# Performance work log

Hardware: AMD Instinct MI355X
Metric: run time of the kernel (lower is better)

Reference implementation:

```python
import jax, jax.numpy as jnp
import numpy as np

N, E, D, H, FF = 50000, 800000, 128, 8, 512
DK = D // H
NTYPES = 5
EPS = 1e-5


def setup_inputs() -> dict:
    key = jax.random.key(0)
    ks = jax.random.split(key, 8)
    x = jax.random.normal(ks[0], (N, D), jnp.float32)
    edges = jax.random.randint(ks[1], (2, E), 0, N)
    etype = jax.random.randint(ks[2], (E,), 0, NTYPES)
    masks = etype[None, :] == jnp.arange(NTYPES)[:, None]  # [5, E] bool, exact partition
    s = 1.0 / np.sqrt(D)
    Wk = jax.random.normal(ks[3], (NTYPES, D, D), jnp.float32) * s
    bk = jnp.zeros((NTYPES, D), jnp.float32)
    ln1_g = jnp.ones((D,), jnp.float32)
    ln1_b = jnp.zeros((D,), jnp.float32)
    ln2_g = jnp.ones((D,), jnp.float32)
    ln2_b = jnp.zeros((D,), jnp.float32)
    W1 = jax.random.normal(ks[4], (D, FF), jnp.float32) * s
    b1 = jnp.zeros((FF,), jnp.float32)
    W2 = jax.random.normal(ks[5], (FF, D), jnp.float32) * (1.0 / np.sqrt(FF))
    b2 = jnp.zeros((D,), jnp.float32)
    return {"x": x, "edges": edges, "masks": masks, "Wk": Wk, "bk": bk,
            "ln1_g": ln1_g, "ln1_b": ln1_b, "ln2_g": ln2_g, "ln2_b": ln2_b,
            "W1": W1, "b1": b1, "W2": W2, "b2": b2}


def _layernorm(x, g, b):
    mu = x.mean(-1, keepdims=True)
    var = x.var(-1, keepdims=True)
    return (x - mu) * jax.lax.rsqrt(var + EPS) * g + b


def _proj(z, idx, masks, W, b):
    # per-edge-type masked linear: output[mask_i] = x[idx[mask_i]] @ W_i + b_i
    g = z[idx]  # [E, D] gather
    out = jnp.zeros((g.shape[0], D), z.dtype)
    for i in range(NTYPES):
        out = out + jnp.where(masks[i][:, None], g @ W[i] + b[i], 0.0)
    return out.reshape(-1, H, DK)  # [E, H, d_k]


def reference(x, edges, masks, Wk, bk, ln1_g, ln1_b, ln2_g, ln2_b, W1, b1, W2, b2):
    src, dst = edges[0], edges[1]
    n = x.shape[0]
    z = _layernorm(x, ln1_g, ln1_b)
    # source module uses self.key projection for query, key AND value
    q = _proj(z, src, masks, Wk, bk)   # [E, H, d_k]
    k = _proj(z, dst, masks, Wk, bk)   # [E, H, d_k]
    v = k                              # value = key(z, edges[1]) == key, reuse
    logits = (q * k).sum(2, keepdims=True)  # [E, H, 1], unscaled as in source
    m = jax.ops.segment_max(jax.lax.stop_gradient(logits), src, num_segments=n)
    scores = jnp.exp(logits - m[src])
    den = jax.ops.segment_sum(scores, src, num_segments=n)
    scores = scores / den[src]
    attn = jax.ops.segment_sum(scores * v, src, num_segments=n).reshape(n, -1)  # [N, D]
    x = x + attn
    z2 = _layernorm(x, ln2_g, ln2_b)
    ff = jax.nn.relu(z2 @ W1 + b1) @ W2 + b2
    return x + ff
```

## Files before the change

### kernel.cpp

```cpp
#include <hip/hip_runtime.h>

#define D 128
#define H 8
#define DK 16
#define FFDIM 512
#define NTYPES 5
#define LN_EPS 1e-5f

typedef __bf16 bf16x8 __attribute__((ext_vector_type(8)));
typedef float f32x4 __attribute__((ext_vector_type(4)));
typedef unsigned short ushort_t;
typedef unsigned int uint_t;

__device__ inline ushort_t bfbits(float f) {
  __bf16 b = (__bf16)f;
  return __builtin_bit_cast(ushort_t, b);
}

__global__ void detect_kernel(const unsigned char* __restrict__ m8, int E,
                              int* __restrict__ flag) {
  int lane = threadIdx.x;
  int s = 1;
  if (lane < E) {
    s = 0;
#pragma unroll
    for (int i = 0; i < NTYPES; ++i) s += (m8[(size_t)i * E + lane] != 0);
  }
  unsigned long long b = __ballot(s == 1);
  if (lane == 0) *flag = (b == ~0ull) ? 1 : 0;
}

__device__ inline int decode_etype(const unsigned char* __restrict__ m8,
                                   int E, int e, int is8) {
  int t = 0;
  if (is8) {
#pragma unroll
    for (int i = 1; i < NTYPES; ++i) t += i * (m8[(size_t)i * E + e] != 0);
  } else {
    const int* m32 = (const int*)m8;
#pragma unroll
    for (int i = 1; i < NTYPES; ++i) t += i * (m32[(size_t)i * E + e] != 0);
  }
  return t > (NTYPES - 1) ? (NTYPES - 1) : t;
}

__global__ __launch_bounds__(256) void ln1_kernel(
    const float* __restrict__ x, const float* __restrict__ g,
    const float* __restrict__ b, ushort_t* __restrict__ zh,
    ushort_t* __restrict__ zl, int n) {
  int row = blockIdx.x * 4 + (threadIdx.x >> 6);
  int lane = threadIdx.x & 63;
  if (row >= n) return;
  const float* xr = x + (size_t)row * D;
  float v0 = xr[lane], v1 = xr[lane + 64];
  float s = v0 + v1, ss = v0 * v0 + v1 * v1;
  for (int o = 32; o; o >>= 1) { s += __shfl_xor(s, o); ss += __shfl_xor(ss, o); }
  float mu = s * (1.f / D);
  float var = ss * (1.f / D) - mu * mu;
  float rs = rsqrtf(var + LN_EPS);
  float z0 = (v0 - mu) * rs * g[lane] + b[lane];
  float z1 = (v1 - mu) * rs * g[lane + 64] + b[lane + 64];
  size_t o0 = (size_t)row * D + lane, o1 = o0 + 64;
  __bf16 h0 = (__bf16)z0, h1 = (__bf16)z1;
  zh[o0] = __builtin_bit_cast(ushort_t, h0);
  zh[o1] = __builtin_bit_cast(ushort_t, h1);
  __bf16 l0 = (__bf16)(z0 - (float)h0), l1 = (__bf16)(z1 - (float)h1);
  zl[o0] = __builtin_bit_cast(ushort_t, l0);
  zl[o1] = __builtin_bit_cast(ushort_t, l1);
}

__global__ void conv_frag_kernel(const float* __restrict__ W,
                                 ushort_t* __restrict__ hi,
                                 int K, int Ncol, size_t matW, size_t matF) {
  int gid = blockIdx.x * 256 + threadIdx.x;
  int total = (Ncol / 16) * (K / 32) * 64;
  if (gid >= total) return;
  const float* Wm = W + (size_t)blockIdx.y * matW;
  ushort_t* him = hi + (size_t)blockIdx.y * matF;
  int l = gid & 63;
  int ck = gid >> 6;
  int kk = ck % (K / 32);
  int c = ck / (K / 32);
  int row0 = kk * 32 + (l >> 4) * 8;
  int col = c * 16 + (l & 15);
  size_t ob = (size_t)gid * 8;
#pragma unroll
  for (int j = 0; j < 8; ++j) {
    float w = Wm[(size_t)(row0 + j) * Ncol + col];
    __bf16 h = (__bf16)w;
    him[ob + j] = __builtin_bit_cast(ushort_t, h);
  }
}

__global__ __launch_bounds__(256, 3) void proj_mfma_kernel(
    const ushort_t* __restrict__ zh, const ushort_t* __restrict__ zl,
    const ushort_t* __restrict__ wkh,
    const float* __restrict__ bk, ushort_t* __restrict__ P, int n) {
  int w = threadIdx.x >> 6, l = threadIdx.x & 63;
  int n0 = blockIdx.x * 64 + w * 16;
  int arow = n0 + (l & 15);
  if (arow >= n) arow = n - 1;
  int koff = (l >> 4) * 8;
  bf16x8 ah[4], al[4];
#pragma unroll
  for (int kk = 0; kk < 4; ++kk) {
    size_t zo = (size_t)arow * D + kk * 32 + koff;
    ah[kk] = *(const bf16x8*)(zh + zo);
    al[kk] = *(const bf16x8*)(zl + zo);
  }
  int col16 = l & 15, rgrp = (l >> 4) * 4;
  for (int t = 0; t < NTYPES; ++t) {
    const ushort_t* bh0 = wkh + (size_t)t * (D * D);
    ushort_t* Pt = P + (size_t)t * n * D;
#pragma unroll
    for (int cp = 0; cp < 4; ++cp) {
      bf16x8 Bh[2][4];
#pragma unroll
      for (int cc = 0; cc < 2; ++cc)
#pragma unroll
        for (int kk = 0; kk < 4; ++kk) {
          size_t o = ((size_t)((cp * 2 + cc) * 4 + kk) * 64 + l) * 8;
          Bh[cc][kk] = *(const bf16x8*)(bh0 + o);
        }
      f32x4 aa[2], ac[2];
#pragma unroll
      for (int cc = 0; cc < 2; ++cc) {
        float bias = bk[t * D + (cp * 2 + cc) * 16 + col16];
        aa[cc] = (f32x4){bias, bias, bias, bias};
        ac[cc] = (f32x4){0.f, 0.f, 0.f, 0.f};
      }
#pragma unroll
      for (int kk = 0; kk < 4; ++kk)
#pragma unroll
        for (int cc = 0; cc < 2; ++cc) {
          aa[cc] = __builtin_amdgcn_mfma_f32_16x16x32_bf16(ah[kk], Bh[cc][kk], aa[cc], 0, 0, 0);
          ac[cc] = __builtin_amdgcn_mfma_f32_16x16x32_bf16(al[kk], Bh[cc][kk], ac[cc], 0, 0, 0);
        }
#pragma unroll
      for (int cc = 0; cc < 2; ++cc)
#pragma unroll
        for (int r = 0; r < 4; ++r) {
          int row = n0 + rgrp + r;
          if (row < n)
            Pt[(size_t)row * D + (cp * 2 + cc) * 16 + col16] =
                bfbits(aa[cc][r] + ac[cc][r]);
        }
    }
  }
}

__global__ void zero_kernel(int* __restrict__ p, int n) {
  int i = blockIdx.x * 256 + threadIdx.x;
  if (i < n) p[i] = 0;
}

__global__ void hist5_kernel(const int* __restrict__ edges,
                             const unsigned char* __restrict__ masks,
                             const int* __restrict__ flag,
                             int* __restrict__ cnt5,
                             unsigned char* __restrict__ etype8, int E) {
  int e = blockIdx.x * 256 + threadIdx.x;
  if (e >= E) return;
  int t = decode_etype(masks, E, e, *flag);
  etype8[e] = (unsigned char)t;
  atomicAdd(&cnt5[edges[e] * 8 + t], 1);
}

__global__ __launch_bounds__(256) void scanA5_kernel(const int* __restrict__ cnt5,
                                                     int* __restrict__ loc,
                                                     int* __restrict__ bsums, int n) {
  __shared__ int ts[256];
  int tid = threadIdx.x;
  int i = blockIdx.x * 256 + tid;
  int v = 0;
  if (i < n) {
    int4 c0 = *(const int4*)(cnt5 + (size_t)i * 8);
    v = c0.x + c0.y + c0.z + c0.w + cnt5[(size_t)i * 8 + 4];
  }
  ts[tid] = v;
  __syncthreads();
  for (int o = 1; o < 256; o <<= 1) {
    int t = (tid >= o) ? ts[tid - o] : 0;
    __syncthreads();
    ts[tid] += t;
    __syncthreads();
  }
  if (i < n) loc[i] = ts[tid] - v;
  if (tid == 255) bsums[blockIdx.x] = ts[255];
}

__global__ __launch_bounds__(256) void scanB_kernel(int* __restrict__ bsums, int nb,
                                                    int* __restrict__ total) {
  __shared__ int ts[256];
  int tid = threadIdx.x;
  int per = (nb + 255) / 256;
  int start = tid * per;
  int end = min(start + per, nb);
  int s = 0;
  for (int i = start; i < end; ++i) s += bsums[i];
  ts[tid] = s;
  __syncthreads();
  for (int o = 1; o < 256; o <<= 1) {
    int t = (tid >= o) ? ts[tid - o] : 0;
    __syncthreads();
    ts[tid] += t;
    __syncthreads();
  }
  int run = ts[tid] - s;
  for (int i = start; i < end; ++i) {
    int v = bsums[i];
    bsums[i] = run;
    run += v;
  }
  if (tid == 255) *total = ts[255];
}

__global__ void scanC_kernel(const int* __restrict__ loc,
                             const int* __restrict__ bsums,
                             const int* __restrict__ total,
                             int* __restrict__ offs, int n) {
  int i = blockIdx.x * 256 + threadIdx.x;
  if (i < n) offs[i] = loc[i] + bsums[i >> 8];
  if (i == 0) offs[n] = *total;
}

__global__ void build5_kernel(const int* __restrict__ offs,
                              const int* __restrict__ cnt5,
                              int* __restrict__ cursor5, int* __restrict__ tb,
                              int n) {
  int i = blockIdx.x * 256 + threadIdx.x;
  if (i >= n) return;
  int base = offs[i];
#pragma unroll
  for (int t = 0; t < NTYPES; ++t) {
    int c = cnt5[(size_t)i * 8 + t];
    cursor5[(size_t)i * 8 + t] = base;
    tb[(size_t)i * 8 + t] = base;
    base += c;
  }
  tb[(size_t)i * 8 + 5] = base;
}

__global__ __launch_bounds__(256) void fill_kernel(
    const int* __restrict__ edges, const unsigned char* __restrict__ etype8,
    int* __restrict__ cursor5, int* __restrict__ elist, int E, int n) {
  int bx = blockIdx.x;
  int range = bx & 7;
  int e = (bx >> 3) * 256 + threadIdx.x;
  if (e >= E) return;
  int per = (n + 7) >> 3;
  int lo = range * per;
  int hi = min(lo + per, n);
  int src = edges[e];
  if (src < lo || src >= hi) return;
  int t = etype8[e];
  int dst = edges[E + e];
  int pos = atomicAdd(&cursor5[src * 8 + t], 1);
  elist[pos] = t * n + dst;
}

__global__ __launch_bounds__(256, 4) void attn_kernel(
    const float* __restrict__ x, const ushort_t* __restrict__ P,
    const int* __restrict__ tb, const int* __restrict__ elist,
    float* __restrict__ out, int n) {
  int node = (blockIdx.x * 256 + threadIdx.x) >> 4;
  int gl = threadIdx.x & 15;
  if (node >= n) return;

  int4 t03 = *(const int4*)(tb + (size_t)node * 8);
  int2 t45 = *(const int2*)(tb + (size_t)node * 8 + 4);
  int bnd0 = t03.x, bnd1 = t03.y, bnd2 = t03.z, bnd3 = t03.w;
  int bnd4 = t45.x, bnd5 = t45.y;

  float m = -1e30f, den = 0.f;
  float a[8];
#pragma unroll
  for (int i = 0; i < 8; ++i) a[i] = 0.f;

#pragma unroll
  for (int t = 0; t < NTYPES; ++t) {
    int jb = (t == 0) ? bnd0 : (t == 1) ? bnd1 : (t == 2) ? bnd2
             : (t == 3) ? bnd3 : bnd4;
    int je = (t == 0) ? bnd1 : (t == 1) ? bnd2 : (t == 2) ? bnd3
             : (t == 3) ? bnd4 : bnd5;
    if (jb >= je) continue;
    bf16x8 qb = *(const bf16x8*)(P + (size_t)(t * n + node) * D + gl * 8);
    float qf[8];
#pragma unroll
    for (int d = 0; d < 8; ++d) qf[d] = (float)qb[d];

    int row = elist[jb];
    bf16x8 kv = *(const bf16x8*)(P + (size_t)row * D + gl * 8);
    for (int j = jb; j < je; ++j) {
      bf16x8 kvn = kv;
      if (j + 1 < je) {
        int rn = elist[j + 1];
        kvn = *(const bf16x8*)(P + (size_t)rn * D + gl * 8);
      }
      float kf[8], p = 0.f;
#pragma unroll
      for (int d = 0; d < 8; ++d) {
        kf[d] = (float)kv[d];
        p += qf[d] * kf[d];
      }
      p += __shfl_xor(p, 1);
      float nm = fmaxf(m, p);
      float sc = __expf(m - nm);
      float w = __expf(p - nm);
      den = den * sc + w;
#pragma unroll
      for (int d = 0; d < 8; ++d) a[d] = a[d] * sc + w * kf[d];
      m = nm;
      kv = kvn;
    }
  }

  float inv = (bnd5 > bnd0) ? 1.f / den : 0.f;
  const float* xr = x + (size_t)node * D + gl * 8;
  float* orow = out + (size_t)node * D + gl * 8;
  float4 xa = *(const float4*)xr;
  float4 xb = *(const float4*)(xr + 4);
  float4 oa, ob;
  oa.x = xa.x + a[0] * inv; oa.y = xa.y + a[1] * inv;
  oa.z = xa.z + a[2] * inv; oa.w = xa.w + a[3] * inv;
  ob.x = xb.x + a[4] * inv; ob.y = xb.y + a[5] * inv;
  ob.z = xb.z + a[6] * inv; ob.w = xb.w + a[7] * inv;
  *(float4*)orow = oa;
  *(float4*)(orow + 4) = ob;
}

__global__ __launch_bounds__(256, 4) void ffn_mfma_kernel(
    const ushort_t* __restrict__ w1h, const ushort_t* __restrict__ w2h,
    const float* __restrict__ b1, const float* __restrict__ b2,
    const float* __restrict__ g, const float* __restrict__ bln,
    float* __restrict__ out, int n) {
  __shared__ ushort_t z2h[32 * D];
  __shared__ ushort_t z2l[32 * D];
  __shared__ float hb2[2][2][16 * 36];
  int tid = threadIdx.x, w = tid >> 6, l = tid & 63;
  int n0 = blockIdx.x * 32;
  int r2 = w >> 1, c2h = w & 1;

  for (int i = w; i < 32; i += 4) {
    int r = n0 + i;
    float v0 = 0.f, v1 = 0.f;
    if (r < n) {
      v0 = out[(size_t)r * D + l];
      v1 = out[(size_t)r * D + 64 + l];
    }
    float s = v0 + v1, ss = v0 * v0 + v1 * v1;
    for (int o = 32; o; o >>= 1) { s += __shfl_xor(s, o); ss += __shfl_xor(ss, o); }
    float mu = s * (1.f / D);
    float var = ss * (1.f / D) - mu * mu;
    float rs = rsqrtf(var + LN_EPS);
    float z0 = (v0 - mu) * rs * g[l] + bln[l];
    float z1 = (v1 - mu) * rs * g[l + 64] + bln[l + 64];
    int sw = (i & 7) << 3;
    int e0 = (i * D + l) ^ sw;
    int e1 = (i * D + l + 64) ^ sw;
    __bf16 h0 = (__bf16)z0, h1 = (__bf16)z1;
    z2h[e0] = __builtin_bit_cast(ushort_t, h0);
    z2h[e1] = __builtin_bit_cast(ushort_t, h1);
    __bf16 l0 = (__bf16)(z0 - (float)h0), l1 = (__bf16)(z1 - (float)h1);
    z2l[e0] = __builtin_bit_cast(ushort_t, l0);
    z2l[e1] = __builtin_bit_cast(ushort_t, l1);
  }
  __syncthreads();

  int lrow = r2 * 16 + (l & 15);
  int koff = (l >> 4) * 8;
  bf16x8 ah[4], al[4];
#pragma unroll
  for (int kk = 0; kk < 4; ++kk) {
    int e = (lrow * D + kk * 32 + koff) ^ ((lrow & 7) << 3);
    ah[kk] = *(const bf16x8*)(z2h + e);
    al[kk] = *(const bf16x8*)(z2l + e);
  }

  int col16 = l & 15, rgrp = (l >> 4) * 4;
  f32x4 acc2[4];
#pragma unroll
  for (int c = 0; c < 4; ++c) acc2[c] = (f32x4){0.f, 0.f, 0.f, 0.f};

  for (int kk2 = 0; kk2 < 16; ++kk2) {
    int c = kk2 * 2 + c2h;
    bf16x8 B1h[4];
#pragma unroll
    for (int kk = 0; kk < 4; ++kk) {
      size_t o = ((size_t)(c * 4 + kk) * 64 + l) * 8;
      B1h[kk] = *(const bf16x8*)(w1h + o);
    }
    float bias = b1[c * 16 + col16];
    f32x4 ha = {bias, bias, bias, bias};
    f32x4 hc = {0.f, 0.f, 0.f, 0.f};
#pragma unroll
    for (int kk = 0; kk < 4; ++kk) {
      ha = __builtin_amdgcn_mfma_f32_16x16x32_bf16(ah[kk], B1h[kk], ha, 0, 0, 0);
      hc = __builtin_amdgcn_mfma_f32_16x16x32_bf16(al[kk], B1h[kk], hc, 0, 0, 0);
    }
    float* hbp = &hb2[kk2 & 1][r2][0];
#pragma unroll
    for (int r = 0; r < 4; ++r)
      hbp[(rgrp + r) * 36 + c2h * 16 + col16] = fmaxf(ha[r] + hc[r], 0.f);
    __syncthreads();
    float av[8];
    const float* hbr = &hb2[kk2 & 1][r2][0];
    *(float4*)&av[0] = *(const float4*)&hbr[(l & 15) * 36 + koff];
    *(float4*)&av[4] = *(const float4*)&hbr[(l & 15) * 36 + koff + 4];
    bf16x8 a2h, a2l;
#pragma unroll
    for (int j = 0; j < 8; ++j) {
      __bf16 hv = (__bf16)av[j];
      a2h[j] = hv;
      a2l[j] = (__bf16)(av[j] - (float)hv);
    }
    bf16x8 B2h[4];
#pragma unroll
    for (int cc2 = 0; cc2 < 4; ++cc2) {
      int ct = c2h * 4 + cc2;
      size_t o = ((size_t)(ct * 16 + kk2) * 64 + l) * 8;
      B2h[cc2] = *(const bf16x8*)(w2h + o);
    }
#pragma unroll
    for (int cc2 = 0; cc2 < 4; ++cc2) {
      acc2[cc2] = __builtin_amdgcn_mfma_f32_16x16x32_bf16(a2h, B2h[cc2], acc2[cc2], 0, 0, 0);
      acc2[cc2] = __builtin_amdgcn_mfma_f32_16x16x32_bf16(a2l, B2h[cc2], acc2[cc2], 0, 0, 0);
    }
  }

#pragma unroll
  for (int cc2 = 0; cc2 < 4; ++cc2) {
    int col = (c2h * 4 + cc2) * 16 + col16;
    float bias2 = b2[col];
#pragma unroll
    for (int r = 0; r < 4; ++r) {
      int row = n0 + r2 * 16 + rgrp + r;
      if (row < n) {
        size_t o = (size_t)row * D + col;
        out[o] = out[o] + acc2[cc2][r] + bias2;
      }
    }
  }
}

extern "C" void kernel_launch(void* const* d_in, const int* in_sizes, int n_in,
                              void* d_out, int out_size, void* d_ws, size_t ws_size,
                              hipStream_t stream) {
  const float* x      = (const float*)d_in[0];
  const int* edges    = (const int*)d_in[1];
  const unsigned char* masks = (const unsigned char*)d_in[2];
  const float* Wk     = (const float*)d_in[3];
  const float* bk     = (const float*)d_in[4];
  const float* ln1_g  = (const float*)d_in[5];
  const float* ln1_b  = (const float*)d_in[6];
  const float* ln2_g  = (const float*)d_in[7];
  const float* ln2_b  = (const float*)d_in[8];
  const float* W1     = (const float*)d_in[9];
  const float* b1     = (const float*)d_in[10];
  const float* W2     = (const float*)d_in[11];
  const float* b2     = (const float*)d_in[12];
  float* out = (float*)d_out;

  const int n = in_sizes[0] / D;
  const int E = in_sizes[1] / 2;
  const int nbn = (n + 255) / 256;

  char* ws = (char*)d_ws;
  size_t off = 0;
  ushort_t* P = (ushort_t*)(ws + off);  off += (size_t)NTYPES * n * D * sizeof(ushort_t);
  int* cnt5   = (int*)(ws + off);       off += (size_t)n * 8 * sizeof(int);
  int* cursor5= (int*)(ws + off);       off += (size_t)n * 8 * sizeof(int);
  int* tb     = (int*)(ws + off);       off += (size_t)n * 8 * sizeof(int);
  int* offs   = (int*)(ws + off);       off += (size_t)(n + 1) * sizeof(int);
  int* loc    = (int*)(ws + off);       off += (size_t)n * sizeof(int);
  int* bsums  = (int*)(ws + off);       off += (size_t)nbn * sizeof(int);
  int* total  = (int*)(ws + off);       off += 64;
  int* elist  = (int*)(ws + off);       off += (size_t)E * sizeof(int);
  unsigned char* etype8 = (unsigned char*)(ws + off); off += (size_t)E + 64;
  int* flag   = (int*)(ws + off);       off += 64;
  ushort_t* wkh = (ushort_t*)(ws + off); off += (size_t)NTYPES * D * D * sizeof(ushort_t);
  ushort_t* w1h = (ushort_t*)(ws + off); off += (size_t)D * FFDIM * sizeof(ushort_t);
  ushort_t* w2h = (ushort_t*)(ws + off); off += (size_t)FFDIM * D * sizeof(ushort_t);
  (void)ws_size; (void)n_in; (void)out_size;

  ushort_t* zh = (ushort_t*)out;
  ushort_t* zl = zh + (size_t)n * D;

  detect_kernel<<<1, 64, 0, stream>>>(masks, E, flag);

  ln1_kernel<<<(n + 3) / 4, 256, 0, stream>>>(x, ln1_g, ln1_b, zh, zl, n);

  {
    dim3 gwk((8 * 4 * 64 + 255) / 256, NTYPES);
    conv_frag_kernel<<<gwk, 256, 0, stream>>>(Wk, wkh, D, D,
                                              (size_t)D * D, (size_t)D * D);
    dim3 gw1(((FFDIM / 16) * 4 * 64 + 255) / 256, 1);
    conv_frag_kernel<<<gw1, 256, 0, stream>>>(W1, w1h, D, FFDIM, 0, 0);
    dim3 gw2((8 * (FFDIM / 32) * 64 + 255) / 256, 1);
    conv_frag_kernel<<<gw2, 256, 0, stream>>>(W2, w2h, FFDIM, D, 0, 0);
  }

  proj_mfma_kernel<<<(n + 63) / 64, 256, 0, stream>>>(zh, zl, wkh, bk, P, n);

  zero_kernel<<<(n * 8 + 255) / 256, 256, 0, stream>>>(cnt5, n * 8);
  hist5_kernel<<<(E + 255) / 256, 256, 0, stream>>>(edges, masks, flag, cnt5, etype8, E);
  scanA5_kernel<<<nbn, 256, 0, stream>>>(cnt5, loc, bsums, n);
  scanB_kernel<<<1, 256, 0, stream>>>(bsums, nbn, total);
  scanC_kernel<<<(n + 255) / 256, 256, 0, stream>>>(loc, bsums, total, offs, n);
  build5_kernel<<<(n + 255) / 256, 256, 0, stream>>>(offs, cnt5, cursor5, tb, n);
  fill_kernel<<<((E + 255) / 256) * 8, 256, 0, stream>>>(edges, etype8, cursor5,
                                                         elist, E, n);

  attn_kernel<<<(n + 15) / 16, 256, 0, stream>>>(x, P, tb, elist, out, n);

  ffn_mfma_kernel<<<(n + 31) / 32, 256, 0, stream>>>(w1h, w2h,
                                                     b1, b2, ln2_g, ln2_b, out, n);
}
```

Measured before the change: 247.9 us.

## Fuse LayerNorm1 into projection, merge scan finalize into build, pipeline FFN W2

LayerNorm1 is now computed inside the projection kernel, which writes the bf16 hi/lo split into swizzled shared memory instead of a global intermediate, removing one kernel and a round trip through global memory. The scanC kernel is folded into build5, which computes offsets directly from loc and bsums. In the FFN kernel, W2 fragment loads and the second-GEMM MFMAs are software-pipelined one step behind the first GEMM, so the W2 loads overlap with the W1 MFMAs. The cost is more shared memory per block (32KB) and a higher occupancy hint on the projection kernel.

```diff
diff --git a/kernel.cpp b/kernel.cpp
--- a/kernel.cpp
+++ b/kernel.cpp
@@ -42,31 +42,6 @@
     for (int i = 1; i < NTYPES; ++i) t += i * (m32[(size_t)i * E + e] != 0);
   }
   return t > (NTYPES - 1) ? (NTYPES - 1) : t;
-}
-
-__global__ __launch_bounds__(256) void ln1_kernel(
-    const float* __restrict__ x, const float* __restrict__ g,
-    const float* __restrict__ b, ushort_t* __restrict__ zh,
-    ushort_t* __restrict__ zl, int n) {
-  int row = blockIdx.x * 4 + (threadIdx.x >> 6);
-  int lane = threadIdx.x & 63;
-  if (row >= n) return;
-  const float* xr = x + (size_t)row * D;
-  float v0 = xr[lane], v1 = xr[lane + 64];
-  float s = v0 + v1, ss = v0 * v0 + v1 * v1;
-  for (int o = 32; o; o >>= 1) { s += __shfl_xor(s, o); ss += __shfl_xor(ss, o); }
-  float mu = s * (1.f / D);
-  float var = ss * (1.f / D) - mu * mu;
-  float rs = rsqrtf(var + LN_EPS);
-  float z0 = (v0 - mu) * rs * g[lane] + b[lane];
-  float z1 = (v1 - mu) * rs * g[lane + 64] + b[lane + 64];
-  size_t o0 = (size_t)row * D + lane, o1 = o0 + 64;
-  __bf16 h0 = (__bf16)z0, h1 = (__bf16)z1;
-  zh[o0] = __builtin_bit_cast(ushort_t, h0);
-  zh[o1] = __builtin_bit_cast(ushort_t, h1);
-  __bf16 l0 = (__bf16)(z0 - (float)h0), l1 = (__bf16)(z1 - (float)h1);
-  zl[o0] = __builtin_bit_cast(ushort_t, l0);
-  zl[o1] = __builtin_bit_cast(ushort_t, l1);
 }
 
 __global__ void conv_frag_kernel(const float* __restrict__ W,
@@ -92,23 +67,53 @@
   }
 }
 
-__global__ __launch_bounds__(256, 3) void proj_mfma_kernel(
-    const ushort_t* __restrict__ zh, const ushort_t* __restrict__ zl,
-    const ushort_t* __restrict__ wkh,
+__global__ __launch_bounds__(256, 4) void projln_kernel(
+    const float* __restrict__ x, const float* __restrict__ g,
+    const float* __restrict__ b, const ushort_t* __restrict__ wkh,
     const float* __restrict__ bk, ushort_t* __restrict__ P, int n) {
-  int w = threadIdx.x >> 6, l = threadIdx.x & 63;
-  int n0 = blockIdx.x * 64 + w * 16;
-  int arow = n0 + (l & 15);
-  if (arow >= n) arow = n - 1;
+  __shared__ ushort_t zsh[64 * D];
+  __shared__ ushort_t zsl[64 * D];
+  int tid = threadIdx.x, w = tid >> 6, l = tid & 63;
+  int n0 = blockIdx.x * 64;
+
+  for (int i = w; i < 64; i += 4) {
+    int r = n0 + i;
+    float v0 = 0.f, v1 = 0.f;
+    if (r < n) {
+      v0 = x[(size_t)r * D + l];
+      v1 = x[(size_t)r * D + 64 + l];
+    }
+    float s = v0 + v1, ss = v0 * v0 + v1 * v1;
+    for (int o = 32; o; o >>= 1) { s += __shfl_xor(s, o); ss += __shfl_xor(ss, o); }
+    float mu = s * (1.f / D);
+    float var = ss * (1.f / D) - mu * mu;
+    float rs = rsqrtf(var + LN_EPS);
+    float z0 = (v0 - mu) * rs * g[l] + b[l];
+    float z1 = (v1 - mu) * rs * g[l + 64] + b[l + 64];
+    int sw = (i & 7) << 3;
+    int e0 = (i * D + l) ^ sw;
+    int e1 = (i * D + l + 64) ^ sw;
+    __bf16 h0 = (__bf16)z0, h1 = (__bf16)z1;
+    zsh[e0] = __builtin_bit_cast(ushort_t, h0);
+    zsh[e1] = __builtin_bit_cast(ushort_t, h1);
+    __bf16 l0 = (__bf16)(z0 - (float)h0), l1 = (__bf16)(z1 - (float)h1);
+    zsl[e0] = __builtin_bit_cast(ushort_t, l0);
+    zsl[e1] = __builtin_bit_cast(ushort_t, l1);
+  }
+  __syncthreads();
+
+  int lrow = w * 16 + (l & 15);
   int koff = (l >> 4) * 8;
   bf16x8 ah[4], al[4];
 #pragma unroll
   for (int kk = 0; kk < 4; ++kk) {
-    size_t zo = (size_t)arow * D + kk * 32 + koff;
-    ah[kk] = *(const bf16x8*)(zh + zo);
-    al[kk] = *(const bf16x8*)(zl + zo);
-  }
+    int e = (lrow * D + kk * 32 + koff) ^ ((lrow & 7) << 3);
+    ah[kk] = *(const bf16x8*)(zsh + e);
+    al[kk] = *(const bf16x8*)(zsl + e);
+  }
+
   int col16 = l & 15, rgrp = (l >> 4) * 4;
+  int rowbase = n0 + w * 16;
   for (int t = 0; t < NTYPES; ++t) {
     const ushort_t* bh0 = wkh + (size_t)t * (D * D);
     ushort_t* Pt = P + (size_t)t * n * D;
@@ -140,7 +145,7 @@
       for (int cc = 0; cc < 2; ++cc)
 #pragma unroll
         for (int r = 0; r < 4; ++r) {
-          int row = n0 + rgrp + r;
+          int row = rowbase + rgrp + r;
           if (row < n)
             Pt[(size_t)row * D + (cp * 2 + cc) * 16 + col16] =
                 bfbits(aa[cc][r] + ac[cc][r]);
@@ -215,22 +220,14 @@
   if (tid == 255) *total = ts[255];
 }
 
-__global__ void scanC_kernel(const int* __restrict__ loc,
-                             const int* __restrict__ bsums,
-                             const int* __restrict__ total,
-                             int* __restrict__ offs, int n) {
-  int i = blockIdx.x * 256 + threadIdx.x;
-  if (i < n) offs[i] = loc[i] + bsums[i >> 8];
-  if (i == 0) offs[n] = *total;
-}
-
-__global__ void build5_kernel(const int* __restrict__ offs,
+__global__ void build5_kernel(const int* __restrict__ loc,
+                              const int* __restrict__ bsums,
                               const int* __restrict__ cnt5,
                               int* __restrict__ cursor5, int* __restrict__ tb,
                               int n) {
   int i = blockIdx.x * 256 + threadIdx.x;
   if (i >= n) return;
-  int base = offs[i];
+  int base = loc[i] + bsums[i >> 8];
 #pragma unroll
   for (int t = 0; t < NTYPES; ++t) {
     int c = cnt5[(size_t)i * 8 + t];
@@ -381,15 +378,36 @@
   f32x4 acc2[4];
 #pragma unroll
   for (int c = 0; c < 4; ++c) acc2[c] = (f32x4){0.f, 0.f, 0.f, 0.f};
-
-  for (int kk2 = 0; kk2 < 16; ++kk2) {
-    int c = kk2 * 2 + c2h;
-    bf16x8 B1h[4];
+  bf16x8 B2prev[4];
+
+#pragma unroll
+  for (int k = 0; k < 16; ++k) {
+    int c = k * 2 + c2h;
+    bf16x8 B1h[4], B2h[4];
 #pragma unroll
     for (int kk = 0; kk < 4; ++kk) {
       size_t o = ((size_t)(c * 4 + kk) * 64 + l) * 8;
       B1h[kk] = *(const bf16x8*)(w1h + o);
     }
+#pragma unroll
+    for (int cc2 = 0; cc2 < 4; ++cc2) {
+      int ct = c2h * 4 + cc2;
+      size_t o = ((size_t)(ct * 16 + k) * 64 + l) * 8;
+      B2h[cc2] = *(const bf16x8*)(w2h + o);
+    }
+    bf16x8 a2h, a2l;
+    if (k > 0) {
+      const float* hbr = &hb2[(k - 1) & 1][r2][0];
+      float av[8];
+      *(float4*)&av[0] = *(const float4*)&hbr[(l & 15) * 36 + koff];
+      *(float4*)&av[4] = *(const float4*)&hbr[(l & 15) * 36 + koff + 4];
+#pragma unroll
+      for (int j = 0; j < 8; ++j) {
+        __bf16 hv = (__bf16)av[j];
+        a2h[j] = hv;
+        a2l[j] = (__bf16)(av[j] - (float)hv);
+      }
+    }
     float bias = b1[c * 16 + col16];
     f32x4 ha = {bias, bias, bias, bias};
     f32x4 hc = {0.f, 0.f, 0.f, 0.f};
@@ -398,13 +416,25 @@
       ha = __builtin_amdgcn_mfma_f32_16x16x32_bf16(ah[kk], B1h[kk], ha, 0, 0, 0);
       hc = __builtin_amdgcn_mfma_f32_16x16x32_bf16(al[kk], B1h[kk], hc, 0, 0, 0);
     }
-    float* hbp = &hb2[kk2 & 1][r2][0];
+    float* hbp = &hb2[k & 1][r2][0];
 #pragma unroll
     for (int r = 0; r < 4; ++r)
       hbp[(rgrp + r) * 36 + c2h * 16 + col16] = fmaxf(ha[r] + hc[r], 0.f);
+    if (k > 0) {
+#pragma unroll
+      for (int cc2 = 0; cc2 < 4; ++cc2) {
+        acc2[cc2] = __builtin_amdgcn_mfma_f32_16x16x32_bf16(a2h, B2prev[cc2], acc2[cc2], 0, 0, 0);
+        acc2[cc2] = __builtin_amdgcn_mfma_f32_16x16x32_bf16(a2l, B2prev[cc2], acc2[cc2], 0, 0, 0);
+      }
+    }
+#pragma unroll
+    for (int cc2 = 0; cc2 < 4; ++cc2) B2prev[cc2] = B2h[cc2];
     __syncthreads();
+  }
+
+  {
+    const float* hbr = &hb2[1][r2][0];
     float av[8];
-    const float* hbr = &hb2[kk2 & 1][r2][0];
     *(float4*)&av[0] = *(const float4*)&hbr[(l & 15) * 36 + koff];
     *(float4*)&av[4] = *(const float4*)&hbr[(l & 15) * 36 + koff + 4];
     bf16x8 a2h, a2l;
@@ -414,17 +444,10 @@
       a2h[j] = hv;
       a2l[j] = (__bf16)(av[j] - (float)hv);
     }
-    bf16x8 B2h[4];
 #pragma unroll
     for (int cc2 = 0; cc2 < 4; ++cc2) {
-      int ct = c2h * 4 + cc2;
-      size_t o = ((size_t)(ct * 16 + kk2) * 64 + l) * 8;
-      B2h[cc2] = *(const bf16x8*)(w2h + o);
-    }
-#pragma unroll
-    for (int cc2 = 0; cc2 < 4; ++cc2) {
-      acc2[cc2] = __builtin_amdgcn_mfma_f32_16x16x32_bf16(a2h, B2h[cc2], acc2[cc2], 0, 0, 0);
-      acc2[cc2] = __builtin_amdgcn_mfma_f32_16x16x32_bf16(a2l, B2h[cc2], acc2[cc2], 0, 0, 0);
+      acc2[cc2] = __builtin_amdgcn_mfma_f32_16x16x32_bf16(a2h, B2prev[cc2], acc2[cc2], 0, 0, 0);
+      acc2[cc2] = __builtin_amdgcn_mfma_f32_16x16x32_bf16(a2l, B2prev[cc2], acc2[cc2], 0, 0, 0);
     }
   }
 
@@ -471,7 +494,6 @@
   int* cnt5   = (int*)(ws + off);       off += (size_t)n * 8 * sizeof(int);
   int* cursor5= (int*)(ws + off);       off += (size_t)n * 8 * sizeof(int);
   int* tb     = (int*)(ws + off);       off += (size_t)n * 8 * sizeof(int);
-  int* offs   = (int*)(ws + off);       off += (size_t)(n + 1) * sizeof(int);
   int* loc    = (int*)(ws + off);       off += (size_t)n * sizeof(int);
   int* bsums  = (int*)(ws + off);       off += (size_t)nbn * sizeof(int);
   int* total  = (int*)(ws + off);       off += 64;
@@ -483,12 +505,7 @@
   ushort_t* w2h = (ushort_t*)(ws + off); off += (size_t)FFDIM * D * sizeof(ushort_t);
   (void)ws_size; (void)n_in; (void)out_size;
 
-  ushort_t* zh = (ushort_t*)out;
-  ushort_t* zl = zh + (size_t)n * D;
-
   detect_kernel<<<1, 64, 0, stream>>>(masks, E, flag);
-
-  ln1_kernel<<<(n + 3) / 4, 256, 0, stream>>>(x, ln1_g, ln1_b, zh, zl, n);
 
   {
     dim3 gwk((8 * 4 * 64 + 255) / 256, NTYPES);
@@ -500,14 +517,13 @@
     conv_frag_kernel<<<gw2, 256, 0, stream>>>(W2, w2h, FFDIM, D, 0, 0);
   }
 
-  proj_mfma_kernel<<<(n + 63) / 64, 256, 0, stream>>>(zh, zl, wkh, bk, P, n);
+  projln_kernel<<<(n + 63) / 64, 256, 0, stream>>>(x, ln1_g, ln1_b, wkh, bk, P, n);
 
   zero_kernel<<<(n * 8 + 255) / 256, 256, 0, stream>>>(cnt5, n * 8);
   hist5_kernel<<<(E + 255) / 256, 256, 0, stream>>>(edges, masks, flag, cnt5, etype8, E);
   scanA5_kernel<<<nbn, 256, 0, stream>>>(cnt5, loc, bsums, n);
   scanB_kernel<<<1, 256, 0, stream>>>(bsums, nbn, total);
-  scanC_kernel<<<(n + 255) / 256, 256, 0, stream>>>(loc, bsums, total, offs, n);
-  build5_kernel<<<(n + 255) / 256, 256, 0, stream>>>(offs, cnt5, cursor5, tb, n);
+  build5_kernel<<<(n + 255) / 256, 256, 0, stream>>>(loc, bsums, cnt5, cursor5, tb, n);
   fill_kernel<<<((E + 255) / 256) * 8, 256, 0, stream>>>(edges, etype8, cursor5,
                                                          elist, E, n);
 
```

Result: faster. 239.2 us (-3.5%).
